# Optimization experiments

Measured on AMD Instinct MI355X. Metric: run time of the kernel, lower is better.

## Reference

```python
import jax, jax.numpy as jnp
import numpy as np

B, S, D = 16, 1024, 64
BASE, SCALE = 10000.0, 1.0


def setup_inputs() -> dict:
    key = jax.random.key(0)
    # geospatial coordinates in [0, 1)
    spa_feat = jax.random.uniform(key, (B, S, 2), dtype=jnp.float32)
    return {"spa_feat": spa_feat}


def reference(spa_feat):
    d = D
    q = d // 4  # number of frequency bands per coordinate axis
    inv_freq = 1.0 / (BASE ** (jnp.arange(q, dtype=jnp.float32) / q))  # [q]
    xy = spa_feat * SCALE                                # [B,S,2]
    freq = xy[..., :, None] * inv_freq                   # [B,S,2,q]
    freq_x, freq_y = freq[..., 0, :], freq[..., 1, :]    # [B,S,q] each
    sin_emb = jnp.concatenate([jnp.sin(freq_x), jnp.sin(freq_y)], axis=-1)  # [B,S,d/2]
    cos_emb = jnp.concatenate([jnp.cos(freq_x), jnp.cos(freq_y)], axis=-1)  # [B,S,d/2]
    b, s, h = sin_emb.shape  # h = d//2 number of 2x2 blocks
    r = 2 * jnp.arange(h)    # top-left row/col index of each 2x2 block
    # Block-diagonal rotation matrix: block i = [[cos_i, -sin_i], [sin_i, cos_i]]
    R = jnp.zeros((b, s, d, d), dtype=sin_emb.dtype)
    R = (R.at[:, :, r, r].set(cos_emb)
           .at[:, :, r, r + 1].set(-sin_emb)
           .at[:, :, r + 1, r].set(sin_emb)
           .at[:, :, r + 1, r + 1].set(cos_emb))
    return R
```

## Files before the change

kernel.cpp:

```cpp
#include <hip/hip_runtime.h>


#define NBS 16384
#define HD  32

__global__ __launch_bounds__(256) void rope2d_kernel(
    const float* __restrict__ spa,
    float* __restrict__ out)
{
    const int bs = blockIdx.x;
    const int t  = threadIdx.x;

    __shared__ float ssin[HD];
    __shared__ float scos[HD];

    if (t < HD) {
        const float xy = spa[bs * 2 + (t >> 4)];
        const int   i  = t & 15;
        const float invf = exp2f(-(float)i * 0.83048202372184059f);
        const float a = xy * invf;
        ssin[t] = sinf(a);
        scos[t] = cosf(a);
    }
    __syncthreads();

    float4* outv = (float4*)out + (size_t)bs * 1024;

    #pragma unroll
    for (int k = 0; k < 4; ++k) {
        const int g    = t + k * 256;
        const int row  = g >> 4;
        const int cg   = g & 15;
        float4 v = make_float4(0.f, 0.f, 0.f, 0.f);
        if (cg == (row >> 2)) {
            const int h = row >> 1;
            const float s = ssin[h];
            const float c = scos[h];
            float e0, e1;
            if (row & 1) { e0 = s; e1 = c; }
            else         { e0 = c; e1 = -s; }
            if (row & 2) { v.z = e0; v.w = e1; }
            else         { v.x = e0; v.y = e1; }
        }
        outv[g] = v;
    }
}

extern "C" void kernel_launch(void* const* d_in, const int* in_sizes, int n_in,
                              void* d_out, int out_size, void* d_ws, size_t ws_size,
                              hipStream_t stream) {
    const float* spa = (const float*)d_in[0];
    float* out = (float*)d_out;
    rope2d_kernel<<<NBS, 256, 0, stream>>>(spa, out);
}
```

Baseline: 253.2 us.

## Process eight positions per block and use nontemporal vector stores

```diff
diff --git a/kernel.cpp b/kernel.cpp
--- a/kernel.cpp
+++ b/kernel.cpp
@@ -2,47 +2,53 @@
 
 
 #define NBS 16384
-#define HD  32
+#define MPB 8
+#define NBLK (NBS / MPB)
+
+typedef float vfloat4 __attribute__((ext_vector_type(4)));
 
 __global__ __launch_bounds__(256) void rope2d_kernel(
     const float* __restrict__ spa,
     float* __restrict__ out)
 {
-    const int bs = blockIdx.x;
-    const int t  = threadIdx.x;
+    const int t   = threadIdx.x;
+    const int bs0 = blockIdx.x * MPB;
 
-    __shared__ float ssin[HD];
-    __shared__ float scos[HD];
+    __shared__ float ssin[MPB * 32];
+    __shared__ float scos[MPB * 32];
 
-    if (t < HD) {
-        const float xy = spa[bs * 2 + (t >> 4)];
-        const int   i  = t & 15;
+    {
+        const int m = t >> 5;
+        const int h = t & 31;
+        const float xy   = spa[(bs0 + m) * 2 + (h >> 4)];
+        const int   i    = h & 15;
         const float invf = exp2f(-(float)i * 0.83048202372184059f);
-        const float a = xy * invf;
-        ssin[t] = sinf(a);
-        scos[t] = cosf(a);
+        float s, c;
+        sincosf(xy * invf, &s, &c);
+        ssin[t] = s;
+        scos[t] = c;
     }
     __syncthreads();
 
-    float4* outv = (float4*)out + (size_t)bs * 1024;
+    vfloat4* outv = (vfloat4*)out + (size_t)bs0 * 1024;
+    const int cg = t & 15;
 
     #pragma unroll
-    for (int k = 0; k < 4; ++k) {
-        const int g    = t + k * 256;
-        const int row  = g >> 4;
-        const int cg   = g & 15;
-        float4 v = make_float4(0.f, 0.f, 0.f, 0.f);
-        if (cg == (row >> 2)) {
+    for (int k = 0; k < 32; ++k) {
+        const int g   = t + k * 256;
+        const int row = (g >> 4) & 63;
+        vfloat4 v = (vfloat4)(0.f, 0.f, 0.f, 0.f);
+        if ((row >> 2) == cg) {
+            const int m = g >> 10;
             const int h = row >> 1;
-            const float s = ssin[h];
-            const float c = scos[h];
-            float e0, e1;
-            if (row & 1) { e0 = s; e1 = c; }
-            else         { e0 = c; e1 = -s; }
+            const float s = ssin[m * 32 + h];
+            const float c = scos[m * 32 + h];
+            const float e0 = (row & 1) ? s : c;
+            const float e1 = (row & 1) ? c : -s;
             if (row & 2) { v.z = e0; v.w = e1; }
             else         { v.x = e0; v.y = e1; }
         }
-        outv[g] = v;
+        __builtin_nontemporal_store(v, &outv[g]);
     }
 }
 
@@ -51,5 +57,5 @@
                               hipStream_t stream) {
     const float* spa = (const float*)d_in[0];
     float* out = (float*)d_out;
-    rope2d_kernel<<<NBS, 256, 0, stream>>>(spa, out);
+    rope2d_kernel<<<NBLK, 256, 0, stream>>>(spa, out);
 }
```

Measured after the change: 265.0 us. 4.6% more time.
